# Performance work log

Hardware: AMD Instinct MI355X
Metric: run time of the kernel (lower is better)

## Reference

```python
import jax, jax.numpy as jnp
import numpy as np

EMB_DIM = 256
Q_DIM = 512
V_DIM = 512

def setup_inputs() -> dict:
    key = jax.random.key(0)
    ks = jax.random.split(key, 7)
    B, S = 8, 2048
    x = jax.random.normal(ks[0], (B, S, EMB_DIM), dtype=jnp.float32)
    s = 1.0 / np.sqrt(EMB_DIM)
    Wq = jax.random.normal(ks[1], (EMB_DIM, Q_DIM), dtype=jnp.float32) * s
    bq = jax.random.normal(ks[2], (Q_DIM,), dtype=jnp.float32) * 0.01
    Wk = jax.random.normal(ks[3], (EMB_DIM, Q_DIM), dtype=jnp.float32) * s
    bk = jax.random.normal(ks[4], (Q_DIM,), dtype=jnp.float32) * 0.01
    Wv = jax.random.normal(ks[5], (EMB_DIM, V_DIM), dtype=jnp.float32) * s
    bv = jax.random.normal(ks[6], (V_DIM,), dtype=jnp.float32) * 0.01
    return {"x": x, "Wq": Wq, "bq": bq, "Wk": Wk, "bk": bk, "Wv": Wv, "bv": bv}

def reference(x, Wq, bq, Wk, bk, Wv, bv):
    # q/k/v projections (torch Linear == x @ W + b with W stored [in, out] here)
    q = jax.nn.sigmoid(jnp.einsum('bse,eq->bsq', x, Wq) + bq)   # [B,S,Q]
    k = jnp.einsum('bse,eq->bsq', x, Wk) + bk                   # [B,S,Q]
    v = jnp.einsum('bse,ev->bsv', x, Wv) + bv                   # [B,S,V]
    scale = 1.0 / jnp.sqrt(jnp.float32(EMB_DIM))
    qk = jnp.einsum('bsq,btq->bst', q, k) * scale               # [B,S,S]
    qk = jax.nn.elu(qk)
    attn = jax.nn.softmax(qk, axis=-1)
    return jnp.einsum('bst,btv->bsv', attn, v)                  # [B,S,V]
```

## Files before the change

kernel.cpp:

```cpp
#include <hip/hip_runtime.h>
#include <hip/hip_bf16.h>
#include <math.h>

typedef unsigned short u16;
using short8 = __attribute__((ext_vector_type(8))) short;
using f32x4  = __attribute__((ext_vector_type(4))) float;

#define BK 32


__device__ __forceinline__ u16 f2bf(float f) {
  union { float f; unsigned u; } v; v.f = f;
  unsigned r = v.u + 0x7FFFu + ((v.u >> 16) & 1u);
  return (u16)(r >> 16);
}

__device__ __forceinline__ float fexp(float x) { return __expf(x); }

__device__ __forceinline__ void gld16(const void* g, void* l) {
  __builtin_amdgcn_global_load_lds(
      (const __attribute__((address_space(1))) void*)g,
      (__attribute__((address_space(3))) void*)l,
      16, 0, 0);
}


__device__ __forceinline__ void gemm_core64(const u16* __restrict__ Ag,
                                            const u16* __restrict__ Bg,
                                            int K, int lda, int ldb,
                                            u16* As, u16* Bs,
                                            f32x4 acc[4][4], int w, int l) {
  const int wm = (w & 1) << 6, wn = (w >> 1) << 6;
  const int ln = l & 15, lq = l >> 4;
  const int sr0 = w * 16 + (l >> 2);
  const int sr1 = 64 + sr0;
  const int skp = (l & 3) * 8;
  const int skg = ((l & 3) ^ ((l >> 3) & 3)) * 8;
  const int kro = (lq ^ ((ln >> 1) & 3)) * 8;

#pragma unroll
  for (int mt = 0; mt < 4; mt++)
#pragma unroll
    for (int nt = 0; nt < 4; nt++) acc[mt][nt] = (f32x4)0.0f;

  for (int k0 = 0; k0 < K; k0 += 64) {
    __syncthreads();
    gld16(Ag + (size_t)sr0 * lda + k0 + skg, As + sr0 * BK + skp);
    gld16(Ag + (size_t)sr1 * lda + k0 + skg, As + sr1 * BK + skp);
    gld16(Ag + (size_t)sr0 * lda + k0 + 32 + skg, As + 4096 + sr0 * BK + skp);
    gld16(Ag + (size_t)sr1 * lda + k0 + 32 + skg, As + 4096 + sr1 * BK + skp);
    gld16(Bg + (size_t)sr0 * ldb + k0 + skg, Bs + sr0 * BK + skp);
    gld16(Bg + (size_t)sr1 * ldb + k0 + skg, Bs + sr1 * BK + skp);
    gld16(Bg + (size_t)sr0 * ldb + k0 + 32 + skg, Bs + 4096 + sr0 * BK + skp);
    gld16(Bg + (size_t)sr1 * ldb + k0 + 32 + skg, Bs + 4096 + sr1 * BK + skp);
    __syncthreads();
#pragma unroll
    for (int h = 0; h < 2; h++) {
      const u16* Ah = As + h * 4096;
      const u16* Bh = Bs + h * 4096;
      short8 af[4], bf[4];
#pragma unroll
      for (int mt = 0; mt < 4; mt++)
        af[mt] = *(const short8*)(Ah + (wm + mt * 16 + ln) * BK + kro);
#pragma unroll
      for (int nt = 0; nt < 4; nt++)
        bf[nt] = *(const short8*)(Bh + (wn + nt * 16 + ln) * BK + kro);
#pragma unroll
      for (int mt = 0; mt < 4; mt++)
#pragma unroll
        for (int nt = 0; nt < 4; nt++)
          acc[mt][nt] = __builtin_amdgcn_mfma_f32_16x16x32_bf16(
              af[mt], bf[nt], acc[mt][nt], 0, 0, 0);
    }
  }
}


__global__ __launch_bounds__(256) void k_conv(
    const float* __restrict__ Wq, const float* __restrict__ Wk,
    const float* __restrict__ Wv, const float* __restrict__ bq,
    const float* __restrict__ bk, const float* __restrict__ bv,
    u16* __restrict__ Wt, float* __restrict__ bcat,
    float* __restrict__ lsum) {
  const int bid = blockIdx.x;
  if (bid < 1536) {
    int i = bid * 256 + threadIdx.x;
    int nn = i >> 8, e = i & 255;
    int sel = nn >> 9, c = nn & 511;
    const float* W = (sel == 0) ? Wq : (sel == 1) ? Wk : Wv;
    Wt[i] = f2bf(W[e * 512 + c]);
    if (e == 0) {
      const float* bb = (sel == 0) ? bq : (sel == 1) ? bk : bv;
      bcat[nn] = bb[c];
    }
  } else {
    int i = (bid - 1536) * 256 + threadIdx.x;
    lsum[i] = 0.0f;
  }
}


__global__ __launch_bounds__(256) void k_proj(
    const float* __restrict__ x, const u16* __restrict__ Wt,
    const float* __restrict__ bcat, u16* __restrict__ qb,
    u16* __restrict__ kb, u16* __restrict__ vtb) {
  __shared__ __align__(16) u16 As8[8 * 4096];
  __shared__ __align__(16) u16 Bs[2 * 4096];
  const int bm = blockIdx.y * 128;
  const int bnq = blockIdx.x;
  const int tid = threadIdx.x, w = tid >> 6, l = tid & 63;
  const int wm = (w & 1) << 6, wn = (w >> 1) << 6;
  const int ln = l & 15, lq = l >> 4;
  const int sr0 = w * 16 + (l >> 2);
  const int sr1 = 64 + sr0;
  const int skp = (l & 3) * 8;
  const int skg = ((l & 3) ^ ((l >> 3) & 3)) * 8;
  const int kro = (lq ^ ((ln >> 1) & 3)) * 8;

#pragma unroll
  for (int kw = 0; kw < 8; kw++) {
    const float* s0 = x + (size_t)(bm + sr0) * 256 + kw * 32 + skg;
    const float* s1 = x + (size_t)(bm + sr1) * 256 + kw * 32 + skg;
    float4 a0 = ((const float4*)s0)[0], a1 = ((const float4*)s0)[1];
    float4 b0 = ((const float4*)s1)[0], b1 = ((const float4*)s1)[1];
    short8 v0, v1;
    ((u16*)&v0)[0] = f2bf(a0.x); ((u16*)&v0)[1] = f2bf(a0.y);
    ((u16*)&v0)[2] = f2bf(a0.z); ((u16*)&v0)[3] = f2bf(a0.w);
    ((u16*)&v0)[4] = f2bf(a1.x); ((u16*)&v0)[5] = f2bf(a1.y);
    ((u16*)&v0)[6] = f2bf(a1.z); ((u16*)&v0)[7] = f2bf(a1.w);
    ((u16*)&v1)[0] = f2bf(b0.x); ((u16*)&v1)[1] = f2bf(b0.y);
    ((u16*)&v1)[2] = f2bf(b0.z); ((u16*)&v1)[3] = f2bf(b0.w);
    ((u16*)&v1)[4] = f2bf(b1.x); ((u16*)&v1)[5] = f2bf(b1.y);
    ((u16*)&v1)[6] = f2bf(b1.z); ((u16*)&v1)[7] = f2bf(b1.w);
    *(short8*)(As8 + kw * 4096 + sr0 * BK + skp) = v0;
    *(short8*)(As8 + kw * 4096 + sr1 * BK + skp) = v1;
  }

  const int b = bm >> 11, t0 = bm & 2047;
  const int cb = bnq * 128;

  for (int p = 0; p < 3; p++) {
    const u16* Bg = Wt + (size_t)(p * 512 + cb) * 256;
    f32x4 acc[4][4];
#pragma unroll
    for (int mt = 0; mt < 4; mt++)
#pragma unroll
      for (int nt = 0; nt < 4; nt++) acc[mt][nt] = (f32x4)0.0f;

#pragma unroll
    for (int it2 = 0; it2 < 4; it2++) {
      __syncthreads();
      gld16(Bg + (size_t)sr0 * 256 + it2 * 64 + skg, Bs + sr0 * BK + skp);
      gld16(Bg + (size_t)sr1 * 256 + it2 * 64 + skg, Bs + sr1 * BK + skp);
      gld16(Bg + (size_t)sr0 * 256 + it2 * 64 + 32 + skg,
            Bs + 4096 + sr0 * BK + skp);
      gld16(Bg + (size_t)sr1 * 256 + it2 * 64 + 32 + skg,
            Bs + 4096 + sr1 * BK + skp);
      __syncthreads();
#pragma unroll
      for (int h = 0; h < 2; h++) {
        const u16* Aw = As8 + (it2 * 2 + h) * 4096;
        const u16* Bh = Bs + h * 4096;
        short8 af[4], bf[4];
#pragma unroll
        for (int mt = 0; mt < 4; mt++)
          af[mt] = *(const short8*)(Aw + (wm + mt * 16 + ln) * BK + kro);
#pragma unroll
        for (int nt = 0; nt < 4; nt++)
          bf[nt] = *(const short8*)(Bh + (wn + nt * 16 + ln) * BK + kro);
#pragma unroll
        for (int mt = 0; mt < 4; mt++)
#pragma unroll
          for (int nt = 0; nt < 4; nt++)
            acc[mt][nt] = __builtin_amdgcn_mfma_f32_16x16x32_bf16(
                af[mt], bf[nt], acc[mt][nt], 0, 0, 0);
      }
    }

    if (p < 2) {
      u16* dst = p ? kb : qb;
#pragma unroll
      for (int mt = 0; mt < 4; mt++)
#pragma unroll
        for (int r = 0; r < 4; r++) {
          int row = bm + wm + mt * 16 + lq * 4 + r;
          ushort4 o;
#pragma unroll
          for (int nt = 0; nt < 4; nt++) {
            int col = wn + nt * 16 + ln;
            float v = acc[mt][nt][r] + bcat[p * 512 + cb + col];
            float ov = (p == 0) ? __builtin_amdgcn_rcpf(1.0f + fexp(-v)) : v;
            ((u16*)&o)[nt] = f2bf(ov);
          }
          *(ushort4*)&dst[(size_t)row * 512 + cb + wn + ln * 4] = o;
        }
    } else {
      u16* tr = As8;
#pragma unroll
      for (int h = 0; h < 2; h++) {
        __syncthreads();
        if ((w & 1) == h) {
#pragma unroll
          for (int mt = 0; mt < 4; mt++)
#pragma unroll
            for (int nt = 0; nt < 4; nt++) {
              int c = wn + nt * 16 + ln;
              float bias = bcat[1024 + cb + c];
#pragma unroll
              for (int r = 0; r < 4; r++) {
                int lr = mt * 16 + lq * 4 + r;
                tr[c * 68 + lr] = f2bf(acc[mt][nt][r] + bias);
              }
            }
        }
        __syncthreads();
        int c2 = tid >> 1, half = tid & 1;
        size_t dbase = ((size_t)b * 512 + cb + c2) * 2048 + t0 + h * 64 + half * 32;
#pragma unroll
        for (int j = 0; j < 4; j++) {
          ushort4 a0 = *(const ushort4*)&tr[c2 * 68 + half * 32 + j * 8];
          ushort4 a1 = *(const ushort4*)&tr[c2 * 68 + half * 32 + j * 8 + 4];
          *(ushort4*)&vtb[dbase + j * 8] = a0;
          *(ushort4*)&vtb[dbase + j * 8 + 4] = a1;
        }
      }
    }
  }
}


__global__ __launch_bounds__(256, 4) void k_qk(const u16* __restrict__ qb,
                                               const u16* __restrict__ kb,
                                               u16* __restrict__ P,
                                               float* __restrict__ lsum) {
  __shared__ __align__(16) u16 As[2 * 4096];
  __shared__ __align__(16) u16 Bs[2 * 4096];
  const int bid = blockIdx.x;
  const int b = bid & 7, t = bid >> 3;
  const int bm = (t >> 4) * 128, bn = (t & 15) * 128;
  const size_t ob = (size_t)b * 2048 * 512;
  const int tid = threadIdx.x, w = tid >> 6, l = tid & 63;
  f32x4 acc[4][4];
  gemm_core64(qb + ob + (size_t)bm * 512, kb + ob + (size_t)bn * 512,
              512, 512, 512, As, Bs, acc, w, l);

  const int wm = (w & 1) << 6, wn = (w >> 1) << 6;
  const int ln = l & 15, lq = l >> 4;
  const float scale = 0.0625f;
#pragma unroll
  for (int mt = 0; mt < 4; mt++)
#pragma unroll
    for (int r = 0; r < 4; r++) {
      int row = bm + wm + mt * 16 + lq * 4 + r;
      float s = 0.0f;
#pragma unroll
      for (int nt = 0; nt < 4; nt++) {
        int col = bn + wn + nt * 16 + ln;
        float v = acc[mt][nt][r] * scale;
        float e = (v > 0.0f) ? v : (fexp(v) - 1.0f);
        float p = fexp(e);
        P[((size_t)b * 2048 + row) * 2048 + col] = f2bf(p);
        s += p;
      }
#pragma unroll
      for (int o = 1; o < 16; o <<= 1) s += __shfl_xor(s, o);
      if (ln == 0) atomicAdd(&lsum[b * 2048 + row], s);
    }
}


__global__ __launch_bounds__(256, 4) void k_pv(const u16* __restrict__ P,
                                               const u16* __restrict__ vtb,
                                               const float* __restrict__ lsum,
                                               float* __restrict__ out) {
  __shared__ __align__(16) u16 As[2 * 4096];
  __shared__ __align__(16) u16 Bs[2 * 4096];
  const int bid = blockIdx.x;
  const int b = bid & 7, t = bid >> 3;
  const int bm = (t >> 2) * 128, bn = (t & 3) * 128;
  const int tid = threadIdx.x, w = tid >> 6, l = tid & 63;
  f32x4 acc[4][4];
  gemm_core64(P  + (size_t)b * 2048 * 2048 + (size_t)bm * 2048,
              vtb + (size_t)b * 512 * 2048 + (size_t)bn * 2048,
              2048, 2048, 2048, As, Bs, acc, w, l);

  const int wm = (w & 1) << 6, wn = (w >> 1) << 6;
  const int ln = l & 15, lq = l >> 4;
#pragma unroll
  for (int mt = 0; mt < 4; mt++)
#pragma unroll
    for (int r = 0; r < 4; r++) {
      int row = bm + wm + mt * 16 + lq * 4 + r;
      float inv = 1.0f / lsum[b * 2048 + row];
#pragma unroll
      for (int nt = 0; nt < 4; nt++) {
        int col = bn + wn + nt * 16 + ln;
        out[((size_t)b * 2048 + row) * 512 + col] = acc[mt][nt][r] * inv;
      }
    }
}


extern "C" void kernel_launch(void* const* d_in, const int* in_sizes, int n_in,
                              void* d_out, int out_size, void* d_ws, size_t ws_size,
                              hipStream_t stream) {
  const float* x  = (const float*)d_in[0];
  const float* Wq = (const float*)d_in[1];
  const float* bq = (const float*)d_in[2];
  const float* Wk = (const float*)d_in[3];
  const float* bk = (const float*)d_in[4];
  const float* Wv = (const float*)d_in[5];
  const float* bv = (const float*)d_in[6];
  float* out = (float*)d_out;
  char* ws = (char*)d_ws;

  u16*  qb   = (u16*)(ws + 0);
  u16*  kb   = (u16*)(ws + 16777216);
  u16*  vtb  = (u16*)(ws + 33554432);
  float* lsum = (float*)(ws + 50331648);
  u16*  P    = (u16*)(ws + 50397184);
  u16*  Wt   = (u16*)(ws + 58785792);
  float* bcat = (float*)(ws + 59572224);

  k_conv<<<1600, 256, 0, stream>>>(Wq, Wk, Wv, bq, bk, bv, Wt, bcat, lsum);
  k_proj<<<dim3(4, 128, 1), 256, 0, stream>>>(x, Wt, bcat, qb, kb, vtb);
  k_qk<<<2048, 256, 0, stream>>>(qb, kb, P, lsum);
  k_pv<<<512, 256, 0, stream>>>(P, vtb, lsum, out);
}
```

Measured before the change: 200.1 us.

## Vectorize P stores via matched column permutation of P and transposed V

The QK kernel now packs each lane's four probability values into one 8-byte store instead of four scattered 2-byte stores. That permutes P's columns inside each 64-wide block. The V-transpose write in the projection kernel applies the same permutation to token order, so the PV product stays correct. The change also adds nontemporal loads for x and nontemporal stores for the output to cut cache pollution. The risk is that P and V fall out of step if either index mapping changes later.

```diff
diff --git a/kernel.cpp b/kernel.cpp
--- a/kernel.cpp
+++ b/kernel.cpp
@@ -119,19 +119,20 @@
 
 #pragma unroll
   for (int kw = 0; kw < 8; kw++) {
-    const float* s0 = x + (size_t)(bm + sr0) * 256 + kw * 32 + skg;
-    const float* s1 = x + (size_t)(bm + sr1) * 256 + kw * 32 + skg;
-    float4 a0 = ((const float4*)s0)[0], a1 = ((const float4*)s0)[1];
-    float4 b0 = ((const float4*)s1)[0], b1 = ((const float4*)s1)[1];
+    const f32x4* s0 = (const f32x4*)(x + (size_t)(bm + sr0) * 256 + kw * 32 + skg);
+    const f32x4* s1 = (const f32x4*)(x + (size_t)(bm + sr1) * 256 + kw * 32 + skg);
+    f32x4 a0 = __builtin_nontemporal_load(s0);
+    f32x4 a1 = __builtin_nontemporal_load(s0 + 1);
+    f32x4 b0 = __builtin_nontemporal_load(s1);
+    f32x4 b1 = __builtin_nontemporal_load(s1 + 1);
     short8 v0, v1;
-    ((u16*)&v0)[0] = f2bf(a0.x); ((u16*)&v0)[1] = f2bf(a0.y);
-    ((u16*)&v0)[2] = f2bf(a0.z); ((u16*)&v0)[3] = f2bf(a0.w);
-    ((u16*)&v0)[4] = f2bf(a1.x); ((u16*)&v0)[5] = f2bf(a1.y);
-    ((u16*)&v0)[6] = f2bf(a1.z); ((u16*)&v0)[7] = f2bf(a1.w);
-    ((u16*)&v1)[0] = f2bf(b0.x); ((u16*)&v1)[1] = f2bf(b0.y);
-    ((u16*)&v1)[2] = f2bf(b0.z); ((u16*)&v1)[3] = f2bf(b0.w);
-    ((u16*)&v1)[4] = f2bf(b1.x); ((u16*)&v1)[5] = f2bf(b1.y);
-    ((u16*)&v1)[6] = f2bf(b1.z); ((u16*)&v1)[7] = f2bf(b1.w);
+#pragma unroll
+    for (int j = 0; j < 4; j++) {
+      ((u16*)&v0)[j]     = f2bf(a0[j]);
+      ((u16*)&v0)[4 + j] = f2bf(a1[j]);
+      ((u16*)&v1)[j]     = f2bf(b0[j]);
+      ((u16*)&v1)[4 + j] = f2bf(b1[j]);
+    }
     *(short8*)(As8 + kw * 4096 + sr0 * BK + skp) = v0;
     *(short8*)(As8 + kw * 4096 + sr1 * BK + skp) = v1;
   }
@@ -195,6 +196,7 @@
           *(ushort4*)&dst[(size_t)row * 512 + cb + wn + ln * 4] = o;
         }
     } else {
+      const int b2 = bm >> 11, t02 = bm & 2047;
       u16* tr = As8;
 #pragma unroll
       for (int h = 0; h < 2; h++) {
@@ -208,14 +210,13 @@
               float bias = bcat[1024 + cb + c];
 #pragma unroll
               for (int r = 0; r < 4; r++) {
-                int lr = mt * 16 + lq * 4 + r;
-                tr[c * 68 + lr] = f2bf(acc[mt][nt][r] + bias);
+                tr[c * 68 + lq * 16 + r * 4 + mt] = f2bf(acc[mt][nt][r] + bias);
               }
             }
         }
         __syncthreads();
         int c2 = tid >> 1, half = tid & 1;
-        size_t dbase = ((size_t)b * 512 + cb + c2) * 2048 + t0 + h * 64 + half * 32;
+        size_t dbase = ((size_t)b2 * 512 + cb + c2) * 2048 + t02 + h * 64 + half * 32;
 #pragma unroll
         for (int j = 0; j < 4; j++) {
           ushort4 a0 = *(const ushort4*)&tr[c2 * 68 + half * 32 + j * 8];
@@ -253,17 +254,18 @@
     for (int r = 0; r < 4; r++) {
       int row = bm + wm + mt * 16 + lq * 4 + r;
       float s = 0.0f;
+      ushort4 o;
 #pragma unroll
       for (int nt = 0; nt < 4; nt++) {
-        int col = bn + wn + nt * 16 + ln;
         float v = acc[mt][nt][r] * scale;
         float e = (v > 0.0f) ? v : (fexp(v) - 1.0f);
         float p = fexp(e);
-        P[((size_t)b * 2048 + row) * 2048 + col] = f2bf(p);
+        ((u16*)&o)[nt] = f2bf(p);
         s += p;
       }
-#pragma unroll
-      for (int o = 1; o < 16; o <<= 1) s += __shfl_xor(s, o);
+      *(ushort4*)&P[((size_t)b * 2048 + row) * 2048 + bn + wn + ln * 4] = o;
+#pragma unroll
+      for (int o2 = 1; o2 < 16; o2 <<= 1) s += __shfl_xor(s, o2);
       if (ln == 0) atomicAdd(&lsum[b * 2048 + row], s);
     }
 }
@@ -295,7 +297,8 @@
 #pragma unroll
       for (int nt = 0; nt < 4; nt++) {
         int col = bn + wn + nt * 16 + ln;
-        out[((size_t)b * 2048 + row) * 512 + col] = acc[mt][nt][r] * inv;
+        __builtin_nontemporal_store(acc[mt][nt][r] * inv,
+            &out[((size_t)b * 2048 + row) * 512 + col]);
       }
     }
 }
```

After: 204.1 us. Within noise of the previous version (+2.0%).
